# Performance work log

Measured on AMD Instinct MI355X. Metric: run time of the kernel, lower is better.

Reference implementation:

```python
import jax, jax.numpy as jnp
import numpy as np

B = 4096   # per-view batch size
D = 256    # projection dim
TEMPERATURE = 0.1
EPS = 1e-12  # F.normalize eps


def setup_inputs() -> dict:
    key = jax.random.key(0)
    kq, kk = jax.random.split(key)
    features_q = jax.random.normal(kq, (B, D), dtype=jnp.float32)
    features_k = jax.random.normal(kk, (B, D), dtype=jnp.float32)
    return {"features_q": features_q, "features_k": features_k}


def _neg_index_matrix(n):
    # Static (numpy) construction of the per-row negative column indices:
    # row i keeps all columns except i (diagonal) and its positive partner.
    rows = np.arange(n)
    partner = (rows + n // 2) % n
    cols = np.broadcast_to(np.arange(n), (n, n))
    keep = (cols != rows[:, None]) & (cols != partner[:, None])
    return cols[keep].reshape(n, n - 2), partner


def reference(features_q, features_k):
    f = jnp.concatenate([features_q, features_k], axis=0)      # [2B, D]
    norm = jnp.maximum(jnp.linalg.norm(f, axis=1, keepdims=True), EPS)
    f = f / norm
    sim = f @ f.T                                              # [2B, 2B]

    n = 2 * B
    neg_idx_np, partner_np = _neg_index_matrix(n)
    rows = jnp.arange(n)
    partner = jnp.asarray(partner_np)
    pos = sim[rows, partner]                                   # [2B]
    neg = jnp.take_along_axis(sim, jnp.asarray(neg_idx_np), axis=1)  # [2B, 2B-2]

    logits = jnp.concatenate([pos[:, None], neg], axis=1) / TEMPERATURE
    # CrossEntropyLoss with label 0 for every row, mean reduction:
    loss = jnp.mean(jax.nn.logsumexp(logits, axis=1) - logits[:, 0])
    return loss
```

## Files before the change

kernel.cpp:

```cpp
#include <hip/hip_runtime.h>
#include <hip/hip_bf16.h>
#include <math.h>

#define N_TOTAL 8192
#define D_DIM   256
#define INV_T   10.0f
#define BM 128
#define BN 128
#define BK 32
#define NT 64

typedef __bf16 bf16_8 __attribute__((ext_vector_type(8)));
typedef float  f32x4  __attribute__((ext_vector_type(4)));

typedef const __attribute__((address_space(1))) unsigned int* gptr_t;
typedef __attribute__((address_space(3))) unsigned int*       lptr_t;

__device__ __forceinline__ void gload16(const void* g, void* l) {
    __builtin_amdgcn_global_load_lds((gptr_t)g, (lptr_t)l, 16, 0, 0);
}

__device__ __forceinline__ unsigned short f2bf(float f) {
    unsigned int u = __float_as_uint(f);
    return (unsigned short)((u + 0x7FFFu + ((u >> 16) & 1u)) >> 16);
}

__global__ __launch_bounds__(256) void normalize_kernel(
    const float* __restrict__ q, const float* __restrict__ k,
    unsigned short* __restrict__ F, float* __restrict__ out)
{
    if (blockIdx.x == 0 && threadIdx.x == 0) out[0] = 0.f;
    int row  = blockIdx.x * 4 + (threadIdx.x >> 6);
    int lane = threadIdx.x & 63;
    const float* src = (row < 4096) ? (q + (size_t)row * D_DIM)
                                    : (k + (size_t)(row - 4096) * D_DIM);
    float4 v = ((const float4*)src)[lane];
    float ss = v.x*v.x + v.y*v.y + v.z*v.z + v.w*v.w;
    #pragma unroll
    for (int off = 32; off > 0; off >>= 1) ss += __shfl_xor(ss, off, 64);
    float inv = 1.0f / fmaxf(sqrtf(ss), 1e-12f);
    ushort4 o;
    o.x = f2bf(v.x * inv); o.y = f2bf(v.y * inv);
    o.z = f2bf(v.z * inv); o.w = f2bf(v.w * inv);
    ((ushort4*)(F + (size_t)row * D_DIM))[lane] = o;
}

__device__ __forceinline__ int tri_off(int x) { return x * NT - (x * (x - 1)) / 2; }

__global__ __launch_bounds__(256) void simloss_gemm(
    const __hip_bfloat16* __restrict__ F,
    float* __restrict__ partial, float* __restrict__ pos)
{
    __shared__ __hip_bfloat16 As[BM * BK];
    __shared__ __hip_bfloat16 Bs[BN * BK];
    __shared__ float s_row[BM];
    __shared__ float s_col[BN];

    int b  = blockIdx.x;
    int bx = (int)(64.5f - sqrtf(64.5f * 64.5f - 2.0f * (float)b));
    if (bx < 0) bx = 0; if (bx > NT - 1) bx = NT - 1;
    while (bx > 0 && tri_off(bx) > b) --bx;
    while (bx < NT - 1 && tri_off(bx + 1) <= b) ++bx;
    const int by = bx + (b - tri_off(bx));
    const bool is_diag = (bx == by);

    const int i0 = bx * BM;
    const int j0 = by * BN;
    const int tid  = threadIdx.x;
    const int wave = tid >> 6;
    const int lane = tid & 63;
    const int wm = (wave & 1) * 64;
    const int wn = (wave >> 1) * 64;
    const int g  = lane >> 4;
    const int cj = lane & 15;

    if (tid < BM) { s_row[tid] = 0.f; s_col[tid] = 0.f; }

    f32x4 acc[4][4];
    #pragma unroll
    for (int a = 0; a < 4; ++a)
        #pragma unroll
        for (int c = 0; c < 4; ++c)
            acc[a][c] = (f32x4){0.f, 0.f, 0.f, 0.f};

    for (int kk = 0; kk < D_DIM; kk += BK) {
        #pragma unroll
        for (int p = 0; p < 2; ++p) {
            gload16(F + (size_t)(i0 + p * 64 + lane) * D_DIM + kk + wave * 8,
                    &As[(wave * 128 + p * 64) * 8]);
            gload16(F + (size_t)(j0 + p * 64 + lane) * D_DIM + kk + wave * 8,
                    &Bs[(wave * 128 + p * 64) * 8]);
        }
        __syncthreads();

        bf16_8 a[4], bfr[4];
        #pragma unroll
        for (int t = 0; t < 4; ++t) {
            a[t]   = *(const bf16_8*)(&As[(g * 128 + wm + t * 16 + cj) * 8]);
            bfr[t] = *(const bf16_8*)(&Bs[(g * 128 + wn + t * 16 + cj) * 8]);
        }
        #pragma unroll
        for (int ti = 0; ti < 4; ++ti)
            #pragma unroll
            for (int tj = 0; tj < 4; ++tj)
                acc[ti][tj] = __builtin_amdgcn_mfma_f32_16x16x32_bf16(
                    a[ti], bfr[tj], acc[ti][tj], 0, 0, 0);
        __syncthreads();
    }

    float colsum[4] = {0.f, 0.f, 0.f, 0.f};
    #pragma unroll
    for (int ti = 0; ti < 4; ++ti) {
        #pragma unroll
        for (int r = 0; r < 4; ++r) {
            const int i = i0 + wm + ti * 16 + g * 4 + r;
            const int partner = (i + 4096) & (N_TOTAL - 1);
            float esum = 0.f;
            #pragma unroll
            for (int tj = 0; tj < 4; ++tj) {
                const int j = j0 + wn + tj * 16 + cj;
                const float v = acc[ti][tj][r];
                float e = __expf(v * INV_T);
                if (is_diag && j == i) e = 0.f;
                if (!is_diag && j == partner) {
                    pos[i] = v; pos[j] = v;
                }
                esum += e;
                colsum[tj] += e;
            }
            #pragma unroll
            for (int off = 1; off < 16; off <<= 1)
                esum += __shfl_xor(esum, off, 64);
            if (cj == 0) atomicAdd(&s_row[wm + ti * 16 + g * 4 + r], esum);
        }
    }
    if (!is_diag) {
        #pragma unroll
        for (int tj = 0; tj < 4; ++tj) {
            float cs = colsum[tj];
            cs += __shfl_xor(cs, 16, 64);
            cs += __shfl_xor(cs, 32, 64);
            if (g == 0) atomicAdd(&s_col[wn + tj * 16 + cj], cs);
        }
    }
    __syncthreads();

    if (tid < BM) {
        partial[(size_t)by * N_TOTAL + i0 + tid] = s_row[tid];
    } else if (!is_diag) {
        partial[(size_t)bx * N_TOTAL + j0 + (tid - BM)] = s_col[tid - BM];
    }
}

__global__ __launch_bounds__(256) void finalize_kernel(
    const float* __restrict__ partial, const float* __restrict__ pos,
    float* __restrict__ out)
{
    const int row = blockIdx.x * 256 + threadIdx.x;
    float s = 0.f;
    #pragma unroll 8
    for (int t = 0; t < NT; ++t)
        s += partial[(size_t)t * N_TOTAL + row];
    float v = logf(s) - pos[row] * INV_T;
    #pragma unroll
    for (int off = 32; off > 0; off >>= 1) v += __shfl_xor(v, off, 64);
    __shared__ float wsum[4];
    if ((threadIdx.x & 63) == 0) wsum[threadIdx.x >> 6] = v;
    __syncthreads();
    if (threadIdx.x == 0)
        atomicAdd(out, (wsum[0] + wsum[1] + wsum[2] + wsum[3]) * (1.0f / N_TOTAL));
}

extern "C" void kernel_launch(void* const* d_in, const int* in_sizes, int n_in,
                              void* d_out, int out_size, void* d_ws, size_t ws_size,
                              hipStream_t stream) {
    const float* q = (const float*)d_in[0];
    const float* k = (const float*)d_in[1];
    float* out = (float*)d_out;

    char* ws = (char*)d_ws;
    const size_t f_bytes = (size_t)N_TOTAL * D_DIM * sizeof(unsigned short);
    const size_t p_bytes = (size_t)NT * N_TOTAL * sizeof(float);
    unsigned short* F = (unsigned short*)ws;
    float* partial = (float*)(ws + f_bytes);
    float* pos     = (float*)(ws + f_bytes + p_bytes);

    normalize_kernel<<<N_TOTAL / 4, 256, 0, stream>>>(q, k, F, out);
    simloss_gemm<<<NT * (NT + 1) / 2, 256, 0, stream>>>((const __hip_bfloat16*)F, partial, pos);
    finalize_kernel<<<32, 256, 0, stream>>>(partial, pos, out);
}
```

Before: 115.8 us.

## Double-buffer LDS tiles to overlap global loads with MFMA compute

```diff
diff --git a/kernel.cpp b/kernel.cpp
--- a/kernel.cpp
+++ b/kernel.cpp
@@ -8,6 +8,7 @@
 #define BM 128
 #define BN 128
 #define BK 32
+#define K_ITERS (D_DIM / BK)
 #define NT 64
 
 typedef __bf16 bf16_8 __attribute__((ext_vector_type(8)));
@@ -51,8 +52,8 @@
     const __hip_bfloat16* __restrict__ F,
     float* __restrict__ partial, float* __restrict__ pos)
 {
-    __shared__ __hip_bfloat16 As[BM * BK];
-    __shared__ __hip_bfloat16 Bs[BN * BK];
+    __shared__ __hip_bfloat16 As[2][BM * BK];
+    __shared__ __hip_bfloat16 Bs[2][BN * BK];
     __shared__ float s_row[BM];
     __shared__ float s_col[BN];
 
@@ -83,21 +84,31 @@
         for (int c = 0; c < 4; ++c)
             acc[a][c] = (f32x4){0.f, 0.f, 0.f, 0.f};
 
-    for (int kk = 0; kk < D_DIM; kk += BK) {
-        #pragma unroll
-        for (int p = 0; p < 2; ++p) {
-            gload16(F + (size_t)(i0 + p * 64 + lane) * D_DIM + kk + wave * 8,
-                    &As[(wave * 128 + p * 64) * 8]);
-            gload16(F + (size_t)(j0 + p * 64 + lane) * D_DIM + kk + wave * 8,
-                    &Bs[(wave * 128 + p * 64) * 8]);
-        }
-        __syncthreads();
+    #define STAGE(buf, kk)                                                        \
+        _Pragma("unroll")                                                         \
+        for (int p = 0; p < 2; ++p) {                                             \
+            gload16(F + (size_t)(i0 + p * 64 + lane) * D_DIM + (kk) + wave * 8,   \
+                    &As[buf][(wave * 128 + p * 64) * 8]);                         \
+            gload16(F + (size_t)(j0 + p * 64 + lane) * D_DIM + (kk) + wave * 8,   \
+                    &Bs[buf][(wave * 128 + p * 64) * 8]);                         \
+        }
+
+    STAGE(0, 0);
+    int cur = 0;
+    for (int kk = 0; kk < K_ITERS; ++kk) {
+        if (kk + 1 < K_ITERS) {
+            STAGE(cur ^ 1, (kk + 1) * BK);
+            asm volatile("s_waitcnt vmcnt(4)" ::: "memory");
+        } else {
+            asm volatile("s_waitcnt vmcnt(0)" ::: "memory");
+        }
+        __builtin_amdgcn_s_barrier();
 
         bf16_8 a[4], bfr[4];
         #pragma unroll
         for (int t = 0; t < 4; ++t) {
-            a[t]   = *(const bf16_8*)(&As[(g * 128 + wm + t * 16 + cj) * 8]);
-            bfr[t] = *(const bf16_8*)(&Bs[(g * 128 + wn + t * 16 + cj) * 8]);
+            a[t]   = *(const bf16_8*)(&As[cur][(g * 128 + wm + t * 16 + cj) * 8]);
+            bfr[t] = *(const bf16_8*)(&Bs[cur][(g * 128 + wn + t * 16 + cj) * 8]);
         }
         #pragma unroll
         for (int ti = 0; ti < 4; ++ti)
@@ -105,8 +116,11 @@
             for (int tj = 0; tj < 4; ++tj)
                 acc[ti][tj] = __builtin_amdgcn_mfma_f32_16x16x32_bf16(
                     a[ti], bfr[tj], acc[ti][tj], 0, 0, 0);
-        __syncthreads();
-    }
+
+        __builtin_amdgcn_s_barrier();
+        cur ^= 1;
+    }
+    #undef STAGE
 
     float colsum[4] = {0.f, 0.f, 0.f, 0.f};
     #pragma unroll
```

Measured after the change: 115.3 us. Within noise of the previous version (-0.5%).
